# Performance work log

Hardware: AMD Instinct MI355X
Metric: run time of the kernel (lower is better)

Reference implementation:

```python
import jax, jax.numpy as jnp
import numpy as np

N_NODES = 50000
N_EDGES = 800000
IN_FEAT = 96
NUM_CLASSES = 40
K_HOPS = 2        # SGConv K=2
LPA_ITERS = 3     # lpaiters


def setup_inputs() -> dict:
    key = jax.random.key(0)
    ks = jax.random.split(key, 6)
    x = jax.random.normal(ks[0], (N_NODES, IN_FEAT), dtype=jnp.float32)
    edge_index = jax.random.randint(ks[1], (2, N_EDGES), 0, N_NODES, dtype=jnp.int64)
    y = jax.random.randint(ks[2], (N_NODES,), 0, NUM_CLASSES, dtype=jnp.int64)
    mask = jax.random.bernoulli(ks[3], 0.5, (N_NODES,))
    edge_weight = jnp.ones((N_EDGES,), dtype=jnp.float32)  # nn.Parameter(torch.ones(num_edges))
    W = jax.random.normal(ks[4], (IN_FEAT, NUM_CLASSES), dtype=jnp.float32) / np.sqrt(IN_FEAT)
    b = jax.random.normal(ks[5], (NUM_CLASSES,), dtype=jnp.float32) * 0.01
    return {"x": x, "edge_index": edge_index, "y": y, "mask": mask,
            "edge_weight": edge_weight, "W": W, "b": b}


def _gcn_norm_self_loops(edge_index, edge_weight, n):
    # PyG gcn_norm with add_self_loops=True (SGConv default), fill_value=1
    row, col = edge_index[0], edge_index[1]
    loop = jnp.arange(n, dtype=row.dtype)
    row = jnp.concatenate([row, loop])
    col = jnp.concatenate([col, loop])
    w = jnp.concatenate([edge_weight, jnp.ones((n,), edge_weight.dtype)])
    deg = jax.ops.segment_sum(w, col, num_segments=n)
    dinv = jnp.where(deg > 0, deg ** -0.5, 0.0)
    return row, col, dinv[row] * w * dinv[col]


def _propagate(h, row, col, w, n):
    # gather -> weight -> scatter-add (aggr='add' at target nodes)
    return jax.ops.segment_sum(w[:, None] * h[row], col, num_segments=n)


def reference(x, edge_index, y, mask, edge_weight, W, b):
    n = x.shape[0]
    # ---- SGConv(K=2) with learnable edge_weight, gcn_norm with self-loops ----
    row, col, norm = _gcn_norm_self_loops(edge_index, edge_weight, n)
    h = x
    for _ in range(K_HOPS):
        h = _propagate(h, row, col, norm, n)
    x_out = h @ W + b
    # ---- LPAconv: edge_weight given, so NO gcn_norm; raw weighted scatter-add ----
    y1h = jax.nn.one_hot(y, NUM_CLASSES, dtype=jnp.float32)
    out = jnp.where(mask[:, None], y1h, 0.0)  # out[mask] = y[mask]
    r2, c2 = edge_index[0], edge_index[1]
    for _ in range(LPA_ITERS):
        out = _propagate(out, r2, c2, edge_weight, n)
    return (x_out, out)
```

## Files before the change

kernel.cpp:

```cpp
#include <hip/hip_runtime.h>
#include <hip/hip_fp16.h>

constexpr int N_NODES     = 50000;
constexpr int N_EDGES     = 800000;
constexpr int IN_FEAT     = 96;
constexpr int NUM_CLASSES = 40;
constexpr int CCH = NUM_CLASSES / 4;
constexpr int CH8 = NUM_CLASSES / 8;
constexpr int HS  = 64;
constexpr int SCAN_B = 1024;
constexpr int NSCAN = (N_NODES + SCAN_B - 1) / SCAN_B;

__device__ __forceinline__ void h8_to_f(const uint4& u, float4& lo, float4& hi) {
    float2 f0 = __half22float2(*reinterpret_cast<const __half2*>(&u.x));
    float2 f1 = __half22float2(*reinterpret_cast<const __half2*>(&u.y));
    float2 f2 = __half22float2(*reinterpret_cast<const __half2*>(&u.z));
    float2 f3 = __half22float2(*reinterpret_cast<const __half2*>(&u.w));
    lo = make_float4(f0.x, f0.y, f1.x, f1.y);
    hi = make_float4(f2.x, f2.y, f3.x, f3.y);
}
__device__ __forceinline__ uint4 f_to_h8(const float4& lo, const float4& hi) {
    uint4 u;
    *reinterpret_cast<__half2*>(&u.x) = __floats2half2_rn(lo.x, lo.y);
    *reinterpret_cast<__half2*>(&u.y) = __floats2half2_rn(lo.z, lo.w);
    *reinterpret_cast<__half2*>(&u.z) = __floats2half2_rn(hi.x, hi.y);
    *reinterpret_cast<__half2*>(&u.w) = __floats2half2_rn(hi.z, hi.w);
    return u;
}

__global__ void rank_k(const int* __restrict__ col, int* __restrict__ cnt,
                       int* __restrict__ rank) {
    int t = blockIdx.x * blockDim.x + threadIdx.x;
    if (t >= N_EDGES / 4) return;
    int4 c = reinterpret_cast<const int4*>(col)[t];
    int4 r;
    r.x = atomicAdd(&cnt[c.x], 1);
    r.y = atomicAdd(&cnt[c.y], 1);
    r.z = atomicAdd(&cnt[c.z], 1);
    r.w = atomicAdd(&cnt[c.w], 1);
    reinterpret_cast<int4*>(rank)[t] = r;
}

__global__ __launch_bounds__(SCAN_B) void scan1_k(const int* __restrict__ cnt,
                                                  int* __restrict__ pscan,
                                                  int* __restrict__ bsum) {
    __shared__ int buf[SCAN_B];
    int tid = threadIdx.x;
    int i = blockIdx.x * SCAN_B + tid;
    int v = (i < N_NODES) ? cnt[i] : 0;
    buf[tid] = v;
    __syncthreads();
    for (int off = 1; off < SCAN_B; off <<= 1) {
        int t = (tid >= off) ? buf[tid - off] : 0;
        __syncthreads();
        buf[tid] += t;
        __syncthreads();
    }
    if (i < N_NODES) pscan[i] = buf[tid] - v;
    if (tid == SCAN_B - 1) bsum[blockIdx.x] = buf[tid];
}

__global__ void scan2_k(const int* __restrict__ bsum, int* __restrict__ boff,
                        int* __restrict__ rowptr) {
    __shared__ int buf[64];
    int tid = threadIdx.x;
    int v = (tid < NSCAN) ? bsum[tid] : 0;
    buf[tid] = v;
    __syncthreads();
    for (int off = 1; off < 64; off <<= 1) {
        int t = (tid >= off) ? buf[tid - off] : 0;
        __syncthreads();
        buf[tid] += t;
        __syncthreads();
    }
    boff[tid] = buf[tid] - v;
    if (tid == NSCAN - 1) rowptr[N_NODES] = buf[tid];
}

__global__ void scan3_k(const int* __restrict__ pscan, const int* __restrict__ boff,
                        int* __restrict__ rowptr) {
    int i = blockIdx.x * blockDim.x + threadIdx.x;
    if (i < N_NODES) rowptr[i] = boff[i >> 10] + pscan[i];
}

__global__ void fill_k(const int* __restrict__ row, const int* __restrict__ col,
                       const float* __restrict__ ew, const int* __restrict__ rowptr,
                       const int* __restrict__ rank, int2* __restrict__ pair) {
    int t = blockIdx.x * blockDim.x + threadIdx.x;
    if (t >= N_EDGES / 4) return;
    int4   c = reinterpret_cast<const int4*>(col)[t];
    int4   r = reinterpret_cast<const int4*>(row)[t];
    int4   k = reinterpret_cast<const int4*>(rank)[t];
    float4 w = reinterpret_cast<const float4*>(ew)[t];
    pair[rowptr[c.x] + k.x] = make_int2(r.x, __float_as_int(w.x));
    pair[rowptr[c.y] + k.y] = make_int2(r.y, __float_as_int(w.y));
    pair[rowptr[c.z] + k.z] = make_int2(r.z, __float_as_int(w.z));
    pair[rowptr[c.w] + k.w] = make_int2(r.w, __float_as_int(w.w));
}

__global__ void node_prep_k(const int* __restrict__ rowptr, const int2* __restrict__ pair,
                            const int* __restrict__ y, const int* __restrict__ mask,
                            float* __restrict__ dinv, int* __restrict__ ym) {
    int i = blockIdx.x * blockDim.x + threadIdx.x;
    if (i >= N_NODES) return;
    int p0 = rowptr[i], p1 = rowptr[i + 1];
    float d = 1.0f;
    for (int p = p0; p < p1; ++p) d += __int_as_float(pair[p].y);
    dinv[i] = d > 0.0f ? rsqrtf(d) : 0.0f;
    ym[i] = (mask[i] != 0) ? y[i] : -1;
}

__global__ __launch_bounds__(256) void xw_k(const float* __restrict__ x,
                                            const float* __restrict__ Wm,
                                            __half* __restrict__ xwh) {
    __shared__ float4 Ws[IN_FEAT * CCH];
    int tid = threadIdx.x;
    for (int t = tid; t < IN_FEAT * CCH; t += 256)
        Ws[t] = reinterpret_cast<const float4*>(Wm)[t];
    __syncthreads();
    int idx = blockIdx.x * 256 + tid;
    if (idx >= N_NODES * CCH) return;
    int i = idx / CCH;
    int j = idx - i * CCH;
    const float4* xr = reinterpret_cast<const float4*>(x + i * IN_FEAT);
    float4 acc = make_float4(0.f, 0.f, 0.f, 0.f);
#pragma unroll
    for (int f4 = 0; f4 < IN_FEAT / 4; ++f4) {
        float4 xv = xr[f4];
        float4 w0 = Ws[(4 * f4 + 0) * CCH + j];
        float4 w1 = Ws[(4 * f4 + 1) * CCH + j];
        float4 w2 = Ws[(4 * f4 + 2) * CCH + j];
        float4 w3 = Ws[(4 * f4 + 3) * CCH + j];
        acc.x = fmaf(xv.x, w0.x, fmaf(xv.y, w1.x, fmaf(xv.z, w2.x, fmaf(xv.w, w3.x, acc.x))));
        acc.y = fmaf(xv.x, w0.y, fmaf(xv.y, w1.y, fmaf(xv.z, w2.y, fmaf(xv.w, w3.y, acc.y))));
        acc.z = fmaf(xv.x, w0.z, fmaf(xv.y, w1.z, fmaf(xv.z, w2.z, fmaf(xv.w, w3.z, acc.z))));
        acc.w = fmaf(xv.x, w0.w, fmaf(xv.y, w1.w, fmaf(xv.z, w2.w, fmaf(xv.w, w3.w, acc.w))));
    }
    uint2 h;
    *reinterpret_cast<__half2*>(&h.x) = __floats2half2_rn(acc.x, acc.y);
    *reinterpret_cast<__half2*>(&h.y) = __floats2half2_rn(acc.z, acc.w);
    reinterpret_cast<uint2*>(xwh + (size_t)i * HS)[j] = h;
}

__global__ void fused1_k(const int* __restrict__ rowptr, const int2* __restrict__ pair,
                         const float* __restrict__ dinv, const int* __restrict__ ym,
                         const __half* __restrict__ xwh,
                         __half* __restrict__ g1h, __half* __restrict__ lAh) {
    int idx = blockIdx.x * blockDim.x + threadIdx.x;
    if (idx >= N_NODES * CH8) return;
    int i = idx / CH8;
    int j = idx - i * CH8;
    int p0 = rowptr[i], p1 = rowptr[i + 1];
    float dc = dinv[i];
    float selfw = dc * dc;
    uint4 vh = *reinterpret_cast<const uint4*>(xwh + (size_t)i * HS + j * 8);
    float4 v0, v1; h8_to_f(vh, v0, v1);
    float4 s0 = make_float4(selfw * v0.x, selfw * v0.y, selfw * v0.z, selfw * v0.w);
    float4 s1 = make_float4(selfw * v1.x, selfw * v1.y, selfw * v1.z, selfw * v1.w);
    float4 a0 = make_float4(0.f, 0.f, 0.f, 0.f);
    float4 a1 = make_float4(0.f, 0.f, 0.f, 0.f);
    int base = j << 3;
    for (int p = p0; p < p1; ++p) {
        int2 pr = pair[p];
        int s = pr.x;
        float w = __int_as_float(pr.y);
        float nv = dinv[s] * (w * dc);
        uint4 uh = *reinterpret_cast<const uint4*>(xwh + (size_t)s * HS + j * 8);
        float4 u0, u1; h8_to_f(uh, u0, u1);
        int t = ym[s] - base;
        s0.x = fmaf(nv, u0.x, s0.x); s0.y = fmaf(nv, u0.y, s0.y);
        s0.z = fmaf(nv, u0.z, s0.z); s0.w = fmaf(nv, u0.w, s0.w);
        s1.x = fmaf(nv, u1.x, s1.x); s1.y = fmaf(nv, u1.y, s1.y);
        s1.z = fmaf(nv, u1.z, s1.z); s1.w = fmaf(nv, u1.w, s1.w);
        a0.x += (t == 0) ? w : 0.f; a0.y += (t == 1) ? w : 0.f;
        a0.z += (t == 2) ? w : 0.f; a0.w += (t == 3) ? w : 0.f;
        a1.x += (t == 4) ? w : 0.f; a1.y += (t == 5) ? w : 0.f;
        a1.z += (t == 6) ? w : 0.f; a1.w += (t == 7) ? w : 0.f;
    }
    *reinterpret_cast<uint4*>(g1h + (size_t)i * HS + j * 8) = f_to_h8(s0, s1);
    *reinterpret_cast<uint4*>(lAh + (size_t)i * HS + j * 8) = f_to_h8(a0, a1);
}

__global__ void fused2_k(const int* __restrict__ rowptr, const int2* __restrict__ pair,
                         const float* __restrict__ dinv,
                         const __half* __restrict__ g1h, const __half* __restrict__ lAh,
                         const float* __restrict__ bias,
                         float* __restrict__ out, __half* __restrict__ lBh) {
    int idx = blockIdx.x * blockDim.x + threadIdx.x;
    if (idx >= N_NODES * CH8) return;
    int i = idx / CH8;
    int j = idx - i * CH8;
    int p0 = rowptr[i], p1 = rowptr[i + 1];
    float dc = dinv[i];
    float selfw = dc * dc;
    uint4 vh = *reinterpret_cast<const uint4*>(g1h + (size_t)i * HS + j * 8);
    float4 v0, v1; h8_to_f(vh, v0, v1);
    float4 s0 = make_float4(selfw * v0.x, selfw * v0.y, selfw * v0.z, selfw * v0.w);
    float4 s1 = make_float4(selfw * v1.x, selfw * v1.y, selfw * v1.z, selfw * v1.w);
    float4 a0 = make_float4(0.f, 0.f, 0.f, 0.f);
    float4 a1 = make_float4(0.f, 0.f, 0.f, 0.f);
    for (int p = p0; p < p1; ++p) {
        int2 pr = pair[p];
        int s = pr.x;
        float w = __int_as_float(pr.y);
        float nv = dinv[s] * (w * dc);
        uint4 uh = *reinterpret_cast<const uint4*>(g1h + (size_t)s * HS + j * 8);
        uint4 mh = *reinterpret_cast<const uint4*>(lAh + (size_t)s * HS + j * 8);
        float4 u0, u1; h8_to_f(uh, u0, u1);
        float4 m0, m1; h8_to_f(mh, m0, m1);
        s0.x = fmaf(nv, u0.x, s0.x); s0.y = fmaf(nv, u0.y, s0.y);
        s0.z = fmaf(nv, u0.z, s0.z); s0.w = fmaf(nv, u0.w, s0.w);
        s1.x = fmaf(nv, u1.x, s1.x); s1.y = fmaf(nv, u1.y, s1.y);
        s1.z = fmaf(nv, u1.z, s1.z); s1.w = fmaf(nv, u1.w, s1.w);
        a0.x = fmaf(w, m0.x, a0.x); a0.y = fmaf(w, m0.y, a0.y);
        a0.z = fmaf(w, m0.z, a0.z); a0.w = fmaf(w, m0.w, a0.w);
        a1.x = fmaf(w, m1.x, a1.x); a1.y = fmaf(w, m1.y, a1.y);
        a1.w = fmaf(w, m1.w, a1.w); a1.z = fmaf(w, m1.z, a1.z);
    }
    const float4* br = reinterpret_cast<const float4*>(bias) + 2 * j;
    float4 b0 = br[0], b1 = br[1];
    s0.x += b0.x; s0.y += b0.y; s0.z += b0.z; s0.w += b0.w;
    s1.x += b1.x; s1.y += b1.y; s1.z += b1.z; s1.w += b1.w;
    float4* oo = reinterpret_cast<float4*>(out + (size_t)i * NUM_CLASSES) + 2 * j;
    oo[0] = s0; oo[1] = s1;
    *reinterpret_cast<uint4*>(lBh + (size_t)i * HS + j * 8) = f_to_h8(a0, a1);
}

__global__ void lpa3_k(const int* __restrict__ rowptr, const int2* __restrict__ pair,
                       const __half* __restrict__ lBh, float* __restrict__ lout) {
    int idx = blockIdx.x * blockDim.x + threadIdx.x;
    if (idx >= N_NODES * CH8) return;
    int i = idx / CH8;
    int j = idx - i * CH8;
    int p0 = rowptr[i], p1 = rowptr[i + 1];
    float4 a0 = make_float4(0.f, 0.f, 0.f, 0.f);
    float4 a1 = make_float4(0.f, 0.f, 0.f, 0.f);
    for (int p = p0; p < p1; ++p) {
        int2 pr = pair[p];
        int s = pr.x;
        float w = __int_as_float(pr.y);
        uint4 mh = *reinterpret_cast<const uint4*>(lBh + (size_t)s * HS + j * 8);
        float4 m0, m1; h8_to_f(mh, m0, m1);
        a0.x = fmaf(w, m0.x, a0.x); a0.y = fmaf(w, m0.y, a0.y);
        a0.z = fmaf(w, m0.z, a0.z); a0.w = fmaf(w, m0.w, a0.w);
        a1.x = fmaf(w, m1.x, a1.x); a1.y = fmaf(w, m1.y, a1.y);
        a1.z = fmaf(w, m1.z, a1.z); a1.w = fmaf(w, m1.w, a1.w);
    }
    float4* lo = reinterpret_cast<float4*>(lout + (size_t)i * NUM_CLASSES) + 2 * j;
    lo[0] = a0; lo[1] = a1;
}


extern "C" void kernel_launch(void* const* d_in, const int* in_sizes, int n_in,
                              void* d_out, int out_size, void* d_ws, size_t ws_size,
                              hipStream_t stream) {
    const float* x    = (const float*)d_in[0];
    const int*   ei   = (const int*)d_in[1];
    const int*   row  = ei;
    const int*   col  = ei + N_EDGES;
    const int*   y    = (const int*)d_in[2];
    const int*   mask = (const int*)d_in[3];
    const float* ew   = (const float*)d_in[4];
    const float* Wm   = (const float*)d_in[5];
    const float* bias = (const float*)d_in[6];
    float* out     = (float*)d_out;
    float* lpa_out = out + N_NODES * NUM_CLASSES;

    int*    cnt    = (int*)d_ws;
    int*    pscan  = cnt + 50000;
    int*    bsum   = pscan + 50048;
    int*    boff   = bsum + 64;
    int*    rowptr = boff + 64;
    int*    rank   = rowptr + 50004;
    int*    ym     = rank + 800000;
    float*  dinv   = (float*)(ym + 50000);
    int2*   pair   = (int2*)(dinv + 50000);
    __half* xwh    = (__half*)(pair + 800000);
    __half* g1h    = xwh + (size_t)N_NODES * HS;
    __half* lAh    = g1h + (size_t)N_NODES * HS;
    __half* lBh    = lAh + (size_t)N_NODES * HS;

    const int B = 256;
    auto g = [](long long n, int b) { return (int)((n + b - 1) / b); };

    hipMemsetAsync(cnt, 0, 50000u * sizeof(int), stream);
    rank_k<<<g(N_EDGES / 4, B), B, 0, stream>>>(col, cnt, rank);
    scan1_k<<<NSCAN, SCAN_B, 0, stream>>>(cnt, pscan, bsum);
    scan2_k<<<1, 64, 0, stream>>>(bsum, boff, rowptr);
    scan3_k<<<g(N_NODES, B), B, 0, stream>>>(pscan, boff, rowptr);
    fill_k<<<g(N_EDGES / 4, B), B, 0, stream>>>(row, col, ew, rowptr, rank, pair);

    node_prep_k<<<g(N_NODES, B), B, 0, stream>>>(rowptr, pair, y, mask, dinv, ym);

    xw_k<<<g((long long)N_NODES * CCH, B), B, 0, stream>>>(x, Wm, xwh);

    fused1_k<<<g((long long)N_NODES * CH8, B), B, 0, stream>>>(
        rowptr, pair, dinv, ym, xwh, g1h, lAh);
    fused2_k<<<g((long long)N_NODES * CH8, B), B, 0, stream>>>(
        rowptr, pair, dinv, g1h, lAh, bias, out, lBh);
    lpa3_k<<<g((long long)N_NODES * CH8, B), B, 0, stream>>>(
        rowptr, pair, lBh, lpa_out);
}
```

Before: 245.2 us.

## Pack per-node dinv and label into feature rows to cut gather transactions

Per-node scalars (dinv and masked label) are packed into the padding of the half-precision feature row, and the first-hop output and LPA state are interleaved in one 256-byte row that also carries dinv. Neighbor gathers then fetch features, label and degree normalization from the same cache lines instead of from separate arrays. The rank kernel also processes eight edges per thread. This relies on node_prep and xw writing disjoint parts of the same row and adds per-row scalar reads on every lane.

```diff
diff --git a/kernel.cpp b/kernel.cpp
--- a/kernel.cpp
+++ b/kernel.cpp
@@ -8,6 +8,8 @@
 constexpr int CCH = NUM_CLASSES / 4;
 constexpr int CH8 = NUM_CLASSES / 8;
 constexpr int HS  = 64;
+constexpr int CS  = 128;
+constexpr int LS  = 64;
 constexpr int SCAN_B = 1024;
 constexpr int NSCAN = (N_NODES + SCAN_B - 1) / SCAN_B;
 
@@ -31,14 +33,20 @@
 __global__ void rank_k(const int* __restrict__ col, int* __restrict__ cnt,
                        int* __restrict__ rank) {
     int t = blockIdx.x * blockDim.x + threadIdx.x;
-    if (t >= N_EDGES / 4) return;
-    int4 c = reinterpret_cast<const int4*>(col)[t];
-    int4 r;
-    r.x = atomicAdd(&cnt[c.x], 1);
-    r.y = atomicAdd(&cnt[c.y], 1);
-    r.z = atomicAdd(&cnt[c.z], 1);
-    r.w = atomicAdd(&cnt[c.w], 1);
-    reinterpret_cast<int4*>(rank)[t] = r;
+    if (t >= N_EDGES / 8) return;
+    int4 c0 = reinterpret_cast<const int4*>(col)[2 * t];
+    int4 c1 = reinterpret_cast<const int4*>(col)[2 * t + 1];
+    int4 r0, r1;
+    r0.x = atomicAdd(&cnt[c0.x], 1);
+    r0.y = atomicAdd(&cnt[c0.y], 1);
+    r0.z = atomicAdd(&cnt[c0.z], 1);
+    r0.w = atomicAdd(&cnt[c0.w], 1);
+    r1.x = atomicAdd(&cnt[c1.x], 1);
+    r1.y = atomicAdd(&cnt[c1.y], 1);
+    r1.z = atomicAdd(&cnt[c1.z], 1);
+    r1.w = atomicAdd(&cnt[c1.w], 1);
+    reinterpret_cast<int4*>(rank)[2 * t]     = r0;
+    reinterpret_cast<int4*>(rank)[2 * t + 1] = r1;
 }
 
 __global__ __launch_bounds__(SCAN_B) void scan1_k(const int* __restrict__ cnt,
@@ -100,19 +108,21 @@
 
 __global__ void node_prep_k(const int* __restrict__ rowptr, const int2* __restrict__ pair,
                             const int* __restrict__ y, const int* __restrict__ mask,
-                            float* __restrict__ dinv, int* __restrict__ ym) {
+                            unsigned short* __restrict__ xwt) {
     int i = blockIdx.x * blockDim.x + threadIdx.x;
     if (i >= N_NODES) return;
     int p0 = rowptr[i], p1 = rowptr[i + 1];
     float d = 1.0f;
     for (int p = p0; p < p1; ++p) d += __int_as_float(pair[p].y);
-    dinv[i] = d > 0.0f ? rsqrtf(d) : 0.0f;
-    ym[i] = (mask[i] != 0) ? y[i] : -1;
+    float dv = d > 0.0f ? rsqrtf(d) : 0.0f;
+    unsigned short* rowp = xwt + (size_t)i * HS;
+    *reinterpret_cast<int*>(rowp + 40)   = (mask[i] != 0) ? y[i] : -1;
+    *reinterpret_cast<float*>(rowp + 42) = dv;
 }
 
 __global__ __launch_bounds__(256) void xw_k(const float* __restrict__ x,
                                             const float* __restrict__ Wm,
-                                            __half* __restrict__ xwh) {
+                                            unsigned short* __restrict__ xwt) {
     __shared__ float4 Ws[IN_FEAT * CCH];
     int tid = threadIdx.x;
     for (int t = tid; t < IN_FEAT * CCH; t += 256)
@@ -139,21 +149,21 @@
     uint2 h;
     *reinterpret_cast<__half2*>(&h.x) = __floats2half2_rn(acc.x, acc.y);
     *reinterpret_cast<__half2*>(&h.y) = __floats2half2_rn(acc.z, acc.w);
-    reinterpret_cast<uint2*>(xwh + (size_t)i * HS)[j] = h;
+    reinterpret_cast<uint2*>(xwt + (size_t)i * HS)[j] = h;
 }
 
 __global__ void fused1_k(const int* __restrict__ rowptr, const int2* __restrict__ pair,
-                         const float* __restrict__ dinv, const int* __restrict__ ym,
-                         const __half* __restrict__ xwh,
-                         __half* __restrict__ g1h, __half* __restrict__ lAh) {
+                         const unsigned short* __restrict__ xwt,
+                         unsigned short* __restrict__ comb) {
     int idx = blockIdx.x * blockDim.x + threadIdx.x;
     if (idx >= N_NODES * CH8) return;
     int i = idx / CH8;
     int j = idx - i * CH8;
     int p0 = rowptr[i], p1 = rowptr[i + 1];
-    float dc = dinv[i];
+    const unsigned short* irow = xwt + (size_t)i * HS;
+    float dc = *reinterpret_cast<const float*>(irow + 42);
     float selfw = dc * dc;
-    uint4 vh = *reinterpret_cast<const uint4*>(xwh + (size_t)i * HS + j * 8);
+    uint4 vh = *reinterpret_cast<const uint4*>(irow + j * 8);
     float4 v0, v1; h8_to_f(vh, v0, v1);
     float4 s0 = make_float4(selfw * v0.x, selfw * v0.y, selfw * v0.z, selfw * v0.w);
     float4 s1 = make_float4(selfw * v1.x, selfw * v1.y, selfw * v1.z, selfw * v1.w);
@@ -164,10 +174,12 @@
         int2 pr = pair[p];
         int s = pr.x;
         float w = __int_as_float(pr.y);
-        float nv = dinv[s] * (w * dc);
-        uint4 uh = *reinterpret_cast<const uint4*>(xwh + (size_t)s * HS + j * 8);
+        const unsigned short* srow = xwt + (size_t)s * HS;
+        uint4 uh = *reinterpret_cast<const uint4*>(srow + j * 8);
+        int   t  = *reinterpret_cast<const int*>(srow + 40) - base;
+        float ds = *reinterpret_cast<const float*>(srow + 42);
+        float nv = ds * (w * dc);
         float4 u0, u1; h8_to_f(uh, u0, u1);
-        int t = ym[s] - base;
         s0.x = fmaf(nv, u0.x, s0.x); s0.y = fmaf(nv, u0.y, s0.y);
         s0.z = fmaf(nv, u0.z, s0.z); s0.w = fmaf(nv, u0.w, s0.w);
         s1.x = fmaf(nv, u1.x, s1.x); s1.y = fmaf(nv, u1.y, s1.y);
@@ -177,23 +189,25 @@
         a1.x += (t == 4) ? w : 0.f; a1.y += (t == 5) ? w : 0.f;
         a1.z += (t == 6) ? w : 0.f; a1.w += (t == 7) ? w : 0.f;
     }
-    *reinterpret_cast<uint4*>(g1h + (size_t)i * HS + j * 8) = f_to_h8(s0, s1);
-    *reinterpret_cast<uint4*>(lAh + (size_t)i * HS + j * 8) = f_to_h8(a0, a1);
+    unsigned short* crow = comb + (size_t)i * CS;
+    *reinterpret_cast<uint4*>(crow + j * 8)      = f_to_h8(s0, s1);
+    *reinterpret_cast<uint4*>(crow + 40 + j * 8) = f_to_h8(a0, a1);
+    if (j == 0) *reinterpret_cast<float*>(crow + 80) = dc;
 }
 
 __global__ void fused2_k(const int* __restrict__ rowptr, const int2* __restrict__ pair,
-                         const float* __restrict__ dinv,
-                         const __half* __restrict__ g1h, const __half* __restrict__ lAh,
+                         const unsigned short* __restrict__ comb,
                          const float* __restrict__ bias,
-                         float* __restrict__ out, __half* __restrict__ lBh) {
+                         float* __restrict__ out, unsigned short* __restrict__ lBh) {
     int idx = blockIdx.x * blockDim.x + threadIdx.x;
     if (idx >= N_NODES * CH8) return;
     int i = idx / CH8;
     int j = idx - i * CH8;
     int p0 = rowptr[i], p1 = rowptr[i + 1];
-    float dc = dinv[i];
+    const unsigned short* irow = comb + (size_t)i * CS;
+    float dc = *reinterpret_cast<const float*>(irow + 80);
     float selfw = dc * dc;
-    uint4 vh = *reinterpret_cast<const uint4*>(g1h + (size_t)i * HS + j * 8);
+    uint4 vh = *reinterpret_cast<const uint4*>(irow + j * 8);
     float4 v0, v1; h8_to_f(vh, v0, v1);
     float4 s0 = make_float4(selfw * v0.x, selfw * v0.y, selfw * v0.z, selfw * v0.w);
     float4 s1 = make_float4(selfw * v1.x, selfw * v1.y, selfw * v1.z, selfw * v1.w);
@@ -203,9 +217,11 @@
         int2 pr = pair[p];
         int s = pr.x;
         float w = __int_as_float(pr.y);
-        float nv = dinv[s] * (w * dc);
-        uint4 uh = *reinterpret_cast<const uint4*>(g1h + (size_t)s * HS + j * 8);
-        uint4 mh = *reinterpret_cast<const uint4*>(lAh + (size_t)s * HS + j * 8);
+        const unsigned short* srow = comb + (size_t)s * CS;
+        uint4 uh = *reinterpret_cast<const uint4*>(srow + j * 8);
+        uint4 mh = *reinterpret_cast<const uint4*>(srow + 40 + j * 8);
+        float ds = *reinterpret_cast<const float*>(srow + 80);
+        float nv = ds * (w * dc);
         float4 u0, u1; h8_to_f(uh, u0, u1);
         float4 m0, m1; h8_to_f(mh, m0, m1);
         s0.x = fmaf(nv, u0.x, s0.x); s0.y = fmaf(nv, u0.y, s0.y);
@@ -215,7 +231,7 @@
         a0.x = fmaf(w, m0.x, a0.x); a0.y = fmaf(w, m0.y, a0.y);
         a0.z = fmaf(w, m0.z, a0.z); a0.w = fmaf(w, m0.w, a0.w);
         a1.x = fmaf(w, m1.x, a1.x); a1.y = fmaf(w, m1.y, a1.y);
-        a1.w = fmaf(w, m1.w, a1.w); a1.z = fmaf(w, m1.z, a1.z);
+        a1.z = fmaf(w, m1.z, a1.z); a1.w = fmaf(w, m1.w, a1.w);
     }
     const float4* br = reinterpret_cast<const float4*>(bias) + 2 * j;
     float4 b0 = br[0], b1 = br[1];
@@ -223,11 +239,11 @@
     s1.x += b1.x; s1.y += b1.y; s1.z += b1.z; s1.w += b1.w;
     float4* oo = reinterpret_cast<float4*>(out + (size_t)i * NUM_CLASSES) + 2 * j;
     oo[0] = s0; oo[1] = s1;
-    *reinterpret_cast<uint4*>(lBh + (size_t)i * HS + j * 8) = f_to_h8(a0, a1);
+    *reinterpret_cast<uint4*>(lBh + (size_t)i * LS + j * 8) = f_to_h8(a0, a1);
 }
 
 __global__ void lpa3_k(const int* __restrict__ rowptr, const int2* __restrict__ pair,
-                       const __half* __restrict__ lBh, float* __restrict__ lout) {
+                       const unsigned short* __restrict__ lBh, float* __restrict__ lout) {
     int idx = blockIdx.x * blockDim.x + threadIdx.x;
     if (idx >= N_NODES * CH8) return;
     int i = idx / CH8;
@@ -239,7 +255,7 @@
         int2 pr = pair[p];
         int s = pr.x;
         float w = __int_as_float(pr.y);
-        uint4 mh = *reinterpret_cast<const uint4*>(lBh + (size_t)s * HS + j * 8);
+        uint4 mh = *reinterpret_cast<const uint4*>(lBh + (size_t)s * LS + j * 8);
         float4 m0, m1; h8_to_f(mh, m0, m1);
         a0.x = fmaf(w, m0.x, a0.x); a0.y = fmaf(w, m0.y, a0.y);
         a0.z = fmaf(w, m0.z, a0.z); a0.w = fmaf(w, m0.w, a0.w);
@@ -266,38 +282,34 @@
     float* out     = (float*)d_out;
     float* lpa_out = out + N_NODES * NUM_CLASSES;
 
-    int*    cnt    = (int*)d_ws;
-    int*    pscan  = cnt + 50000;
-    int*    bsum   = pscan + 50048;
-    int*    boff   = bsum + 64;
-    int*    rowptr = boff + 64;
-    int*    rank   = rowptr + 50004;
-    int*    ym     = rank + 800000;
-    float*  dinv   = (float*)(ym + 50000);
-    int2*   pair   = (int2*)(dinv + 50000);
-    __half* xwh    = (__half*)(pair + 800000);
-    __half* g1h    = xwh + (size_t)N_NODES * HS;
-    __half* lAh    = g1h + (size_t)N_NODES * HS;
-    __half* lBh    = lAh + (size_t)N_NODES * HS;
+    unsigned short* xwt  = (unsigned short*)d_ws;
+    unsigned short* comb = xwt + (size_t)N_NODES * HS;
+    unsigned short* lBh  = comb + (size_t)N_NODES * CS;
+    int2* pair  = (int2*)(lBh + (size_t)N_NODES * LS);
+    int* wsi    = (int*)(pair + N_EDGES);
+    int* cnt    = wsi;
+    int* pscan  = cnt + 50000;
+    int* bsum   = pscan + 50048;
+    int* boff   = bsum + 64;
+    int* rowptr = boff + 64;
+    int* rank   = rowptr + 50004;
 
     const int B = 256;
     auto g = [](long long n, int b) { return (int)((n + b - 1) / b); };
 
     hipMemsetAsync(cnt, 0, 50000u * sizeof(int), stream);
-    rank_k<<<g(N_EDGES / 4, B), B, 0, stream>>>(col, cnt, rank);
+    rank_k<<<g(N_EDGES / 8, B), B, 0, stream>>>(col, cnt, rank);
     scan1_k<<<NSCAN, SCAN_B, 0, stream>>>(cnt, pscan, bsum);
     scan2_k<<<1, 64, 0, stream>>>(bsum, boff, rowptr);
     scan3_k<<<g(N_NODES, B), B, 0, stream>>>(pscan, boff, rowptr);
     fill_k<<<g(N_EDGES / 4, B), B, 0, stream>>>(row, col, ew, rowptr, rank, pair);
 
-    node_prep_k<<<g(N_NODES, B), B, 0, stream>>>(rowptr, pair, y, mask, dinv, ym);
-
-    xw_k<<<g((long long)N_NODES * CCH, B), B, 0, stream>>>(x, Wm, xwh);
-
-    fused1_k<<<g((long long)N_NODES * CH8, B), B, 0, stream>>>(
-        rowptr, pair, dinv, ym, xwh, g1h, lAh);
-    fused2_k<<<g((long long)N_NODES * CH8, B), B, 0, stream>>>(
-        rowptr, pair, dinv, g1h, lAh, bias, out, lBh);
-    lpa3_k<<<g((long long)N_NODES * CH8, B), B, 0, stream>>>(
-        rowptr, pair, lBh, lpa_out);
-}
+    node_prep_k<<<g(N_NODES, B), B, 0, stream>>>(rowptr, pair, y, mask, xwt);
+
+    xw_k<<<g((long long)N_NODES * CCH, B), B, 0, stream>>>(x, Wm, xwt);
+
+    fused1_k<<<g((long long)N_NODES * CH8, B), B, 0, stream>>>(rowptr, pair, xwt, comb);
+    fused2_k<<<g((long long)N_NODES * CH8, B), B, 0, stream>>>(rowptr, pair, comb,
+                                                              bias, out, lBh);
+    lpa3_k<<<g((long long)N_NODES * CH8, B), B, 0, stream>>>(rowptr, pair, lBh, lpa_out);
+}
```

Result: no change. 241.3 us (-1.6%).
